# Kernel tuning notes

Measured on AMD Instinct MI355X. Metric: run time of the kernel, lower is better.

The kernel has to match this reference:

```python
import jax, jax.numpy as jnp
import numpy as np
from jax import lax

B, T, D, I, K = 16, 2048, 512, 1024, 31

def setup_inputs() -> dict:
    key = jax.random.key(0)
    ks = jax.random.split(key, 5)
    x = jax.random.normal(ks[0], (B, T, D), dtype=jnp.float32)
    ln_g = jnp.ones((D,), jnp.float32)
    ln_b = jnp.zeros((D,), jnp.float32)
    w1 = jax.random.normal(ks[1], (2 * I, D), dtype=jnp.float32) * 0.02
    b1 = jnp.zeros((2 * I,), jnp.float32)
    dw = jax.random.normal(ks[2], (I, 1, K), dtype=jnp.float32) * 0.1
    dwb = jnp.zeros((I,), jnp.float32)
    alpha = jnp.full((I,), 0.25, jnp.float32)  # PReLU default init
    w2 = jax.random.normal(ks[3], (D, I), dtype=jnp.float32) * 0.02
    b2 = jnp.zeros((D,), jnp.float32)
    return {"x": x, "ln_g": ln_g, "ln_b": ln_b, "w1": w1, "b1": b1,
            "dw": dw, "dwb": dwb, "alpha": alpha, "w2": w2, "b2": b2}

def reference(x, ln_g, ln_b, w1, b1, dw, dwb, alpha, w2, b2):
    # LayerNorm over last dim
    mu = jnp.mean(x, axis=-1, keepdims=True)
    var = jnp.mean(jnp.square(x - mu), axis=-1, keepdims=True)
    xn = (x - mu) * lax.rsqrt(var + 1e-5) * ln_g + ln_b
    # pointwise conv D -> 2I (1x1 conv == GEMM over channels)
    h = jnp.einsum('btd,ed->bte', xn, w1) + b1            # [B,T,2I]
    a, g = jnp.split(h, 2, axis=-1)                       # chunk on channel dim
    u = a * jax.nn.silu(g)                                # SwiGLU [B,T,I]
    # depthwise conv, kernel 31, same padding 15
    uc = jnp.transpose(u, (0, 2, 1))                      # [B,I,T]
    pad = K // 2
    v = lax.conv_general_dilated(uc, dw, window_strides=(1,),
                                 padding=[(pad, pad)],
                                 dimension_numbers=('NCH', 'OIH', 'NCH'),
                                 feature_group_count=I)
    v = v + dwb[None, :, None]
    # PReLU per channel
    v = jnp.where(v > 0, v, alpha[None, :, None] * v)
    # pointwise conv I -> D, then back to [B,T,D]
    out = jnp.einsum('bct,dc->btd', v, w2) + b2
    return out
```

## Files before the change

### kernel.cpp

```cpp
#include <hip/hip_runtime.h>
#include <hip/hip_bf16.h>
#include <stdint.h>

#define B_  16
#define T_  2048
#define D_  512
#define I_  1024
#define K_  31
#define M_  (B_ * T_)

typedef __attribute__((ext_vector_type(8))) __bf16 bf16x8;
typedef __attribute__((ext_vector_type(4))) float  f32x4;

__device__ __forceinline__ unsigned short f2bf(float f) {
    union { float f; uint32_t u; } v; v.f = f;
    uint32_t u = v.u;
    uint32_t r = (u + 0x7FFFu + ((u >> 16) & 1u)) >> 16;
    return (unsigned short)r;
}
__device__ __forceinline__ float bf2f(unsigned short h) {
    union { uint32_t u; float f; } v; v.u = ((uint32_t)h) << 16;
    return v.f;
}

__device__ __forceinline__ void gload_lds16(const void* g, void* l) {
    __builtin_amdgcn_global_load_lds(
        (const __attribute__((address_space(1))) unsigned int*)g,
        (__attribute__((address_space(3))) unsigned int*)l, 16, 0, 0);
}

__global__ __launch_bounds__(256) void prep_weights(
    const float* __restrict__ w1, const float* __restrict__ w2,
    unsigned short* __restrict__ w1b, unsigned short* __restrict__ w2b)
{
    int i = blockIdx.x * 256 + threadIdx.x;
    const int n1 = 2 * I_ * D_;
    const int n2 = D_ * I_;
    if (i < n1) w1b[i] = f2bf(w1[i]);
    if (i < n2) w2b[i] = f2bf(w2[i]);
}

__global__ __launch_bounds__(256) void ln_kernel(
    const float* __restrict__ x, const float* __restrict__ gam,
    const float* __restrict__ bet, unsigned short* __restrict__ xn)
{
    int row  = blockIdx.x * 4 + (threadIdx.x >> 6);
    int lane = threadIdx.x & 63;
    const float* xr = x + (size_t)row * D_ + lane * 8;
    float4 a0 = *(const float4*)xr;
    float4 a1 = *(const float4*)(xr + 4);
    float xs[8] = {a0.x, a0.y, a0.z, a0.w, a1.x, a1.y, a1.z, a1.w};

    float s = xs[0]+xs[1]+xs[2]+xs[3]+xs[4]+xs[5]+xs[6]+xs[7];
    #pragma unroll
    for (int off = 32; off; off >>= 1) s += __shfl_xor(s, off);
    float mu = s * (1.0f / D_);

    float q = 0.f;
    #pragma unroll
    for (int j = 0; j < 8; ++j) { float d = xs[j] - mu; q += d * d; }
    #pragma unroll
    for (int off = 32; off; off >>= 1) q += __shfl_xor(q, off);
    float rstd = rsqrtf(q * (1.0f / D_) + 1e-5f);

    float4 g0 = *(const float4*)(gam + lane * 8);
    float4 g1 = *(const float4*)(gam + lane * 8 + 4);
    float4 e0 = *(const float4*)(bet + lane * 8);
    float4 e1 = *(const float4*)(bet + lane * 8 + 4);
    float gs[8] = {g0.x, g0.y, g0.z, g0.w, g1.x, g1.y, g1.z, g1.w};
    float bs[8] = {e0.x, e0.y, e0.z, e0.w, e1.x, e1.y, e1.z, e1.w};

    unsigned short o[8];
    #pragma unroll
    for (int j = 0; j < 8; ++j) o[j] = f2bf((xs[j] - mu) * rstd * gs[j] + bs[j]);
    uint4 pk;
    pk.x = (uint32_t)o[0] | ((uint32_t)o[1] << 16);
    pk.y = (uint32_t)o[2] | ((uint32_t)o[3] << 16);
    pk.z = (uint32_t)o[4] | ((uint32_t)o[5] << 16);
    pk.w = (uint32_t)o[6] | ((uint32_t)o[7] << 16);
    *(uint4*)(xn + (size_t)row * D_ + lane * 8) = pk;
}


#define PRE_() do { \
    __builtin_amdgcn_s_barrier(); \
    asm volatile("s_waitcnt lgkmcnt(0)" ::: "memory"); \
    __builtin_amdgcn_sched_barrier(0); \
    __builtin_amdgcn_s_setprio(1); } while (0)

#define POST0_() do { \
    __builtin_amdgcn_s_setprio(0); \
    __builtin_amdgcn_sched_barrier(0); \
    __builtin_amdgcn_s_barrier(); } while (0)

#define POSTV_(six) do { \
    __builtin_amdgcn_s_setprio(0); \
    __builtin_amdgcn_sched_barrier(0); \
    if (six) asm volatile("s_waitcnt vmcnt(6)" ::: "memory"); \
    else     asm volatile("s_waitcnt vmcnt(0)" ::: "memory"); \
    __builtin_amdgcn_s_barrier(); } while (0)

#define POSTW_(two) do { \
    __builtin_amdgcn_s_setprio(0); \
    __builtin_amdgcn_sched_barrier(0); \
    if (two) asm volatile("s_waitcnt vmcnt(2)" ::: "memory"); \
    __builtin_amdgcn_s_barrier(); } while (0)

#define RD(base, idx) (*(const bf16x8*)(lds + (base) + (idx) * 2048))
#define MF(m, n, a, b) \
    acc[m][n] = __builtin_amdgcn_mfma_f32_16x16x32_bf16(a, b, acc[m][n], 0, 0, 0)

#define ISSUE_A(j, c) do { \
    gload_lds16(agA[j], lds + (c) * 65536 + tid * 16 + (j) * 8192); \
    agA[j] += 64; } while (0)
#define ISSUE_B(j, c) do { \
    gload_lds16(agB[j], lds + (c) * 65536 + 32768 + tid * 16 + (j) * 8192); \
    agB[j] += 64; } while (0)
#define ISSUE6(c) do { ISSUE_B(0,c); ISSUE_B(1,c); ISSUE_B(2,c); ISSUE_B(3,c); \
                       ISSUE_A(0,c); ISSUE_A(2,c); } while (0)
#define ISSUE2(c) do { ISSUE_A(1,c); ISSUE_A(3,c); } while (0)

#define KTILE(CUR, NXT, DOISS, VM6) do { \
    bf16x8 af0, af1, af2, af3, bb0, bb1, bb2, bb3; \
    bb0 = RD(bB0[CUR],0); bb1 = RD(bB0[CUR],1); bb2 = RD(bB0[CUR],2); bb3 = RD(bB0[CUR],3); \
    af0 = RD(bA0[CUR],0); af1 = RD(bA0[CUR],1); af2 = RD(bA0[CUR],2); af3 = RD(bA0[CUR],3); \
    if (DOISS) { ISSUE6(NXT); } \
    PRE_(); \
    MF(0,0,af0,bb0); MF(0,1,af0,bb1); MF(0,2,af0,bb2); MF(0,3,af0,bb3); \
    MF(1,0,af1,bb0); MF(1,1,af1,bb1); MF(1,2,af1,bb2); MF(1,3,af1,bb3); \
    MF(2,0,af2,bb0); MF(2,1,af2,bb1); MF(2,2,af2,bb2); MF(2,3,af2,bb3); \
    MF(3,0,af3,bb0); MF(3,1,af3,bb1); MF(3,2,af3,bb2); MF(3,3,af3,bb3); \
    POSTV_(VM6); \
    af0 = RD(bA0[CUR],4); af1 = RD(bA0[CUR],5); af2 = RD(bA0[CUR],6); af3 = RD(bA0[CUR],7); \
    if (DOISS) { ISSUE2(NXT); } \
    PRE_(); \
    MF(4,0,af0,bb0); MF(4,1,af0,bb1); MF(4,2,af0,bb2); MF(4,3,af0,bb3); \
    MF(5,0,af1,bb0); MF(5,1,af1,bb1); MF(5,2,af1,bb2); MF(5,3,af1,bb3); \
    MF(6,0,af2,bb0); MF(6,1,af2,bb1); MF(6,2,af2,bb2); MF(6,3,af2,bb3); \
    MF(7,0,af3,bb0); MF(7,1,af3,bb1); MF(7,2,af3,bb2); MF(7,3,af3,bb3); \
    POST0_(); \
    bb0 = RD(bB1[CUR],0); bb1 = RD(bB1[CUR],1); bb2 = RD(bB1[CUR],2); bb3 = RD(bB1[CUR],3); \
    af0 = RD(bA1[CUR],0); af1 = RD(bA1[CUR],1); af2 = RD(bA1[CUR],2); af3 = RD(bA1[CUR],3); \
    PRE_(); \
    MF(0,0,af0,bb0); MF(0,1,af0,bb1); MF(0,2,af0,bb2); MF(0,3,af0,bb3); \
    MF(1,0,af1,bb0); MF(1,1,af1,bb1); MF(1,2,af1,bb2); MF(1,3,af1,bb3); \
    MF(2,0,af2,bb0); MF(2,1,af2,bb1); MF(2,2,af2,bb2); MF(2,3,af2,bb3); \
    MF(3,0,af3,bb0); MF(3,1,af3,bb1); MF(3,2,af3,bb2); MF(3,3,af3,bb3); \
    POST0_(); \
    af0 = RD(bA1[CUR],4); af1 = RD(bA1[CUR],5); af2 = RD(bA1[CUR],6); af3 = RD(bA1[CUR],7); \
    PRE_(); \
    MF(4,0,af0,bb0); MF(4,1,af0,bb1); MF(4,2,af0,bb2); MF(4,3,af0,bb3); \
    MF(5,0,af1,bb0); MF(5,1,af1,bb1); MF(5,2,af1,bb2); MF(5,3,af1,bb3); \
    MF(6,0,af2,bb0); MF(6,1,af2,bb1); MF(6,2,af2,bb2); MF(6,3,af2,bb3); \
    MF(7,0,af3,bb0); MF(7,1,af3,bb1); MF(7,2,af3,bb2); MF(7,3,af3,bb3); \
    POSTW_(DOISS); \
} while (0)

__global__ __launch_bounds__(512, 2) void gemm1_kernel(
    const unsigned short* __restrict__ xn,
    const unsigned short* __restrict__ w1b,
    const float* __restrict__ b1,
    unsigned short* __restrict__ u)
{
    __shared__ __align__(16) unsigned char lds[131072];
    const int tid  = threadIdx.x;
    const int lane = tid & 63;
    const int wv   = tid >> 6;
    const int wm   = wv >> 2;
    const int wn   = wv & 3;

    const int bid = blockIdx.x;
    const int sw  = (bid & 7) * 128 + (bid >> 3);
    const int jb  = sw & 7;
    const int m0  = (sw >> 3) * 256;

    const unsigned short* agA[4];
    const unsigned short* agB[4];
    {
        const int srow = tid >> 3;
        const int scb  = tid & 7;
        #pragma unroll
        for (int j = 0; j < 4; ++j) {
            int row = j * 64 + srow;
            int kk  = (scb ^ (row & 7)) * 8;
            agA[j] = xn + (size_t)(m0 + row) * D_ + kk;
            int chl  = ((row >> 5) << 4) + (row & 15);
            int wrow = ((row & 16) ? 1024 : 0) + jb * 128 + chl;
            agB[j] = w1b + (size_t)wrow * D_ + kk;
        }
    }

    const int l15 = lane & 15;
    const unsigned kq  = (unsigned)((lane >> 4) << 4);
    const unsigned swx = (unsigned)((l15 & 7) << 4);
    const unsigned rA  = (unsigned)(wm * 128 + l15) * 128;
    const unsigned rB  = 32768u + (unsigned)(wn * 64 + l15) * 128;
    const unsigned bA0[2] = {rA + (kq ^ swx),          rA + (kq ^ swx) + 65536u};
    const unsigned bA1[2] = {rA + ((64u + kq) ^ swx),  rA + ((64u + kq) ^ swx) + 65536u};
    const unsigned bB0[2] = {rB + (kq ^ swx),          rB + (kq ^ swx) + 65536u};
    const unsigned bB1[2] = {rB + ((64u + kq) ^ swx),  rB + ((64u + kq) ^ swx) + 65536u};

    f32x4 acc[8][4];
    #pragma unroll
    for (int i = 0; i < 8; ++i)
        #pragma unroll
        for (int n = 0; n < 4; ++n) acc[i][n] = (f32x4){0.f, 0.f, 0.f, 0.f};

    ISSUE6(0); ISSUE2(0);
    asm volatile("s_waitcnt vmcnt(2)" ::: "memory");
    __builtin_amdgcn_s_barrier();

    const int NT = D_ / 64;
    for (int tt = 0; tt < NT; tt += 2) {
        KTILE(0, 1, true, true);
        const bool more = (tt + 2 < NT);
        KTILE(1, 0, more, more);
    }

    const int rQ = (lane >> 4) * 4;
    #pragma unroll
    for (int p = 0; p < 2; ++p) {
        int ch = jb * 128 + wn * 32 + p * 16 + l15;
        float ba = b1[ch];
        float bg = b1[1024 + ch];
        #pragma unroll
        for (int mf = 0; mf < 8; ++mf) {
            #pragma unroll
            for (int r = 0; r < 4; ++r) {
                float a = acc[mf][2 * p][r] + ba;
                float g = acc[mf][2 * p + 1][r] + bg;
                float sg = g / (1.0f + __expf(-g));
                int row = m0 + wm * 128 + mf * 16 + rQ + r;
                u[(size_t)row * I_ + ch] = f2bf(a * sg);
            }
        }
    }
}

__global__ __launch_bounds__(256) void dwconv_kernel(
    const unsigned short* __restrict__ u, const float* __restrict__ dw,
    const float* __restrict__ dwb, const float* __restrict__ alpha,
    unsigned short* __restrict__ v)
{
    __shared__ __align__(16) unsigned short su[286][64];
    const int tid     = threadIdx.x;
    const int c0      = blockIdx.y * 64;
    const int b       = blockIdx.z;
    const int tile_t0 = blockIdx.x * 256;

    #pragma unroll
    for (int it = 0; it < 9; ++it) {
        int r = it * 32 + (tid >> 3);
        if (r < 286) {
            int tt = tile_t0 - 15 + r;
            int cc = (tid & 7) * 8;
            uint4 val = {0u, 0u, 0u, 0u};
            if (tt >= 0 && tt < T_)
                val = *(const uint4*)(u + ((size_t)b * T_ + tt) * I_ + c0 + cc);
            *(uint4*)(&su[r][cc]) = val;
        }
    }
    __syncthreads();

    const int c  = tid & 63;
    const int tb = (tid >> 6) * 64;

    float dwk[K_];
    #pragma unroll
    for (int k = 0; k < K_; ++k) dwk[k] = dw[(c0 + c) * K_ + k];
    const float bia = dwb[c0 + c], al = alpha[c0 + c];

    unsigned short* vb = v + ((size_t)b * T_ + tile_t0 + tb) * I_ + c0 + c;

    #pragma unroll
    for (int chk = 0; chk < 4; ++chk) {
        float w[46];
        #pragma unroll
        for (int j = 0; j < 46; ++j)
            w[j] = bf2f(su[tb + chk * 16 + j][c]);
        #pragma unroll
        for (int i = 0; i < 16; ++i) {
            float acc = bia;
            #pragma unroll
            for (int k = 0; k < K_; ++k) acc += w[i + k] * dwk[k];
            float o = acc > 0.f ? acc : al * acc;
            vb[(size_t)(chk * 16 + i) * I_] = f2bf(o);
        }
    }
}

__global__ __launch_bounds__(512, 2) void gemm2_kernel(
    const unsigned short* __restrict__ v,
    const unsigned short* __restrict__ w2b,
    const float* __restrict__ b2,
    float* __restrict__ out)
{
    __shared__ __align__(16) unsigned char lds[131072];
    const int tid  = threadIdx.x;
    const int lane = tid & 63;
    const int wv   = tid >> 6;
    const int wm   = wv >> 2;
    const int wn   = wv & 3;

    const int bid = blockIdx.x;
    const int sw  = (bid & 7) * 32 + (bid >> 3);
    const int n0  = (sw & 1) * 256;
    const int m0  = (sw >> 1) * 256;

    const unsigned short* agA[4];
    const unsigned short* agB[4];
    {
        const int srow = tid >> 3;
        const int scb  = tid & 7;
        #pragma unroll
        for (int j = 0; j < 4; ++j) {
            int row = j * 64 + srow;
            int kk  = (scb ^ (row & 7)) * 8;
            agA[j] = v   + (size_t)(m0 + row) * I_ + kk;
            agB[j] = w2b + (size_t)(n0 + row) * I_ + kk;
        }
    }

    const int l15 = lane & 15;
    const unsigned kq  = (unsigned)((lane >> 4) << 4);
    const unsigned swx = (unsigned)((l15 & 7) << 4);
    const unsigned rA  = (unsigned)(wm * 128 + l15) * 128;
    const unsigned rB  = 32768u + (unsigned)(wn * 64 + l15) * 128;
    const unsigned bA0[2] = {rA + (kq ^ swx),          rA + (kq ^ swx) + 65536u};
    const unsigned bA1[2] = {rA + ((64u + kq) ^ swx),  rA + ((64u + kq) ^ swx) + 65536u};
    const unsigned bB0[2] = {rB + (kq ^ swx),          rB + (kq ^ swx) + 65536u};
    const unsigned bB1[2] = {rB + ((64u + kq) ^ swx),  rB + ((64u + kq) ^ swx) + 65536u};

    f32x4 acc[8][4];
    #pragma unroll
    for (int i = 0; i < 8; ++i)
        #pragma unroll
        for (int n = 0; n < 4; ++n) acc[i][n] = (f32x4){0.f, 0.f, 0.f, 0.f};

    ISSUE6(0); ISSUE2(0);
    asm volatile("s_waitcnt vmcnt(2)" ::: "memory");
    __builtin_amdgcn_s_barrier();

    const int NT = I_ / 64;
    for (int tt = 0; tt < NT; tt += 2) {
        KTILE(0, 1, true, true);
        const bool more = (tt + 2 < NT);
        KTILE(1, 0, more, more);
    }

    const int rQ = (lane >> 4) * 4;
    #pragma unroll
    for (int nf = 0; nf < 4; ++nf) {
        int col = n0 + wn * 64 + nf * 16 + l15;
        float bb = b2[col];
        #pragma unroll
        for (int mf = 0; mf < 8; ++mf) {
            #pragma unroll
            for (int r = 0; r < 4; ++r) {
                int row = m0 + wm * 128 + mf * 16 + rQ + r;
                out[(size_t)row * D_ + col] = acc[mf][nf][r] + bb;
            }
        }
    }
}

extern "C" void kernel_launch(void* const* d_in, const int* in_sizes, int n_in,
                              void* d_out, int out_size, void* d_ws, size_t ws_size,
                              hipStream_t stream) {
    const float* x     = (const float*)d_in[0];
    const float* ln_g  = (const float*)d_in[1];
    const float* ln_b  = (const float*)d_in[2];
    const float* w1    = (const float*)d_in[3];
    const float* b1    = (const float*)d_in[4];
    const float* dw    = (const float*)d_in[5];
    const float* dwb   = (const float*)d_in[6];
    const float* alpha = (const float*)d_in[7];
    const float* w2    = (const float*)d_in[8];
    const float* b2    = (const float*)d_in[9];
    float* out = (float*)d_out;

    char* ws = (char*)d_ws;
    unsigned short* xn  = (unsigned short*)(ws);
    unsigned short* u   = (unsigned short*)(ws + 33554432);
    unsigned short* v   = (unsigned short*)(ws + 100663296);
    unsigned short* w1b = (unsigned short*)(ws + 167772160);
    unsigned short* w2b = (unsigned short*)(ws + 169869312);

    prep_weights<<<4096, 256, 0, stream>>>(w1, w2, w1b, w2b);
    ln_kernel<<<M_ / 4, 256, 0, stream>>>(x, ln_g, ln_b, xn);
    gemm1_kernel<<<(M_ / 256) * (I_ / 128), 512, 0, stream>>>(xn, w1b, b1, u);
    dim3 gc(T_ / 256, I_ / 64, B_);
    dwconv_kernel<<<gc, 256, 0, stream>>>(u, dw, dwb, alpha, v);
    gemm2_kernel<<<(M_ / 256) * (D_ / 256), 512, 0, stream>>>(v, w2b, b2, out);
}
```

Baseline: 214.6 us.

## Make GEMM kernels persistent over output tiles and drop intra-tile barriers

gemm1 now launches 256 blocks, and each block loops over four output column tiles. The global-to-LDS prefetch of the next tile's K slices is issued during the current tile's last steps, so loads run across tile boundaries. Inside each K-tile the per-quarter s_barrier calls are removed, leaving only two barriers per K-tile, and the SiLU divide is replaced with a hardware reciprocal. This cuts launch and prologue overhead and synchronization stalls, at the risk of LDS read/write races from the reduced barriers and fewer blocks for load balance.

```diff
diff --git a/kernel.cpp b/kernel.cpp
--- a/kernel.cpp
+++ b/kernel.cpp
@@ -82,33 +82,17 @@
 }
 
 
-#define PRE_() do { \
-    __builtin_amdgcn_s_barrier(); \
-    asm volatile("s_waitcnt lgkmcnt(0)" ::: "memory"); \
-    __builtin_amdgcn_sched_barrier(0); \
-    __builtin_amdgcn_s_setprio(1); } while (0)
-
-#define POST0_() do { \
-    __builtin_amdgcn_s_setprio(0); \
-    __builtin_amdgcn_sched_barrier(0); \
-    __builtin_amdgcn_s_barrier(); } while (0)
-
-#define POSTV_(six) do { \
-    __builtin_amdgcn_s_setprio(0); \
-    __builtin_amdgcn_sched_barrier(0); \
-    if (six) asm volatile("s_waitcnt vmcnt(6)" ::: "memory"); \
-    else     asm volatile("s_waitcnt vmcnt(0)" ::: "memory"); \
-    __builtin_amdgcn_s_barrier(); } while (0)
-
-#define POSTW_(two) do { \
-    __builtin_amdgcn_s_setprio(0); \
-    __builtin_amdgcn_sched_barrier(0); \
-    if (two) asm volatile("s_waitcnt vmcnt(2)" ::: "memory"); \
-    __builtin_amdgcn_s_barrier(); } while (0)
+#define VMCNT(n) asm volatile("s_waitcnt vmcnt(" #n ")" ::: "memory")
 
 #define RD(base, idx) (*(const bf16x8*)(lds + (base) + (idx) * 2048))
 #define MF(m, n, a, b) \
     acc[m][n] = __builtin_amdgcn_mfma_f32_16x16x32_bf16(a, b, acc[m][n], 0, 0, 0)
+#define MFQ(MB, x0, x1, x2, x3, c0, c1, c2, c3) do { \
+    MF(MB+0,0,x0,c0); MF(MB+0,1,x0,c1); MF(MB+0,2,x0,c2); MF(MB+0,3,x0,c3); \
+    MF(MB+1,0,x1,c0); MF(MB+1,1,x1,c1); MF(MB+1,2,x1,c2); MF(MB+1,3,x1,c3); \
+    MF(MB+2,0,x2,c0); MF(MB+2,1,x2,c1); MF(MB+2,2,x2,c2); MF(MB+2,3,x2,c3); \
+    MF(MB+3,0,x3,c0); MF(MB+3,1,x3,c1); MF(MB+3,2,x3,c2); MF(MB+3,3,x3,c3); \
+} while (0)
 
 #define ISSUE_A(j, c) do { \
     gload_lds16(agA[j], lds + (c) * 65536 + tid * 16 + (j) * 8192); \
@@ -120,40 +104,38 @@
                        ISSUE_A(0,c); ISSUE_A(2,c); } while (0)
 #define ISSUE2(c) do { ISSUE_A(1,c); ISSUE_A(3,c); } while (0)
 
-#define KTILE(CUR, NXT, DOISS, VM6) do { \
-    bf16x8 af0, af1, af2, af3, bb0, bb1, bb2, bb3; \
-    bb0 = RD(bB0[CUR],0); bb1 = RD(bB0[CUR],1); bb2 = RD(bB0[CUR],2); bb3 = RD(bB0[CUR],3); \
-    af0 = RD(bA0[CUR],0); af1 = RD(bA0[CUR],1); af2 = RD(bA0[CUR],2); af3 = RD(bA0[CUR],3); \
+#define LGKM_SCHED() do { \
+    asm volatile("s_waitcnt lgkmcnt(0)" ::: "memory"); \
+    __builtin_amdgcn_sched_barrier(0); } while (0)
+
+#define KTILE2(CUR, NXT, DOISS) do { \
+    bf16x8 b0,b1,b2,b3, x0,x1,x2,x3; \
+    b0 = RD(bB0[CUR],0); b1 = RD(bB0[CUR],1); b2 = RD(bB0[CUR],2); b3 = RD(bB0[CUR],3); \
+    x0 = RD(bA0[CUR],0); x1 = RD(bA0[CUR],1); x2 = RD(bA0[CUR],2); x3 = RD(bA0[CUR],3); \
     if (DOISS) { ISSUE6(NXT); } \
-    PRE_(); \
-    MF(0,0,af0,bb0); MF(0,1,af0,bb1); MF(0,2,af0,bb2); MF(0,3,af0,bb3); \
-    MF(1,0,af1,bb0); MF(1,1,af1,bb1); MF(1,2,af1,bb2); MF(1,3,af1,bb3); \
-    MF(2,0,af2,bb0); MF(2,1,af2,bb1); MF(2,2,af2,bb2); MF(2,3,af2,bb3); \
-    MF(3,0,af3,bb0); MF(3,1,af3,bb1); MF(3,2,af3,bb2); MF(3,3,af3,bb3); \
-    POSTV_(VM6); \
-    af0 = RD(bA0[CUR],4); af1 = RD(bA0[CUR],5); af2 = RD(bA0[CUR],6); af3 = RD(bA0[CUR],7); \
+    __builtin_amdgcn_s_setprio(1); \
+    MFQ(0, x0,x1,x2,x3, b0,b1,b2,b3); \
+    __builtin_amdgcn_s_setprio(0); \
+    LGKM_SCHED(); \
+    if (DOISS) { VMCNT(6); } else { VMCNT(0); } \
+    __builtin_amdgcn_s_barrier(); \
+    x0 = RD(bA0[CUR],4); x1 = RD(bA0[CUR],5); x2 = RD(bA0[CUR],6); x3 = RD(bA0[CUR],7); \
     if (DOISS) { ISSUE2(NXT); } \
-    PRE_(); \
-    MF(4,0,af0,bb0); MF(4,1,af0,bb1); MF(4,2,af0,bb2); MF(4,3,af0,bb3); \
-    MF(5,0,af1,bb0); MF(5,1,af1,bb1); MF(5,2,af1,bb2); MF(5,3,af1,bb3); \
-    MF(6,0,af2,bb0); MF(6,1,af2,bb1); MF(6,2,af2,bb2); MF(6,3,af2,bb3); \
-    MF(7,0,af3,bb0); MF(7,1,af3,bb1); MF(7,2,af3,bb2); MF(7,3,af3,bb3); \
-    POST0_(); \
-    bb0 = RD(bB1[CUR],0); bb1 = RD(bB1[CUR],1); bb2 = RD(bB1[CUR],2); bb3 = RD(bB1[CUR],3); \
-    af0 = RD(bA1[CUR],0); af1 = RD(bA1[CUR],1); af2 = RD(bA1[CUR],2); af3 = RD(bA1[CUR],3); \
-    PRE_(); \
-    MF(0,0,af0,bb0); MF(0,1,af0,bb1); MF(0,2,af0,bb2); MF(0,3,af0,bb3); \
-    MF(1,0,af1,bb0); MF(1,1,af1,bb1); MF(1,2,af1,bb2); MF(1,3,af1,bb3); \
-    MF(2,0,af2,bb0); MF(2,1,af2,bb1); MF(2,2,af2,bb2); MF(2,3,af2,bb3); \
-    MF(3,0,af3,bb0); MF(3,1,af3,bb1); MF(3,2,af3,bb2); MF(3,3,af3,bb3); \
-    POST0_(); \
-    af0 = RD(bA1[CUR],4); af1 = RD(bA1[CUR],5); af2 = RD(bA1[CUR],6); af3 = RD(bA1[CUR],7); \
-    PRE_(); \
-    MF(4,0,af0,bb0); MF(4,1,af0,bb1); MF(4,2,af0,bb2); MF(4,3,af0,bb3); \
-    MF(5,0,af1,bb0); MF(5,1,af1,bb1); MF(5,2,af1,bb2); MF(5,3,af1,bb3); \
-    MF(6,0,af2,bb0); MF(6,1,af2,bb1); MF(6,2,af2,bb2); MF(6,3,af2,bb3); \
-    MF(7,0,af3,bb0); MF(7,1,af3,bb1); MF(7,2,af3,bb2); MF(7,3,af3,bb3); \
-    POSTW_(DOISS); \
+    __builtin_amdgcn_s_setprio(1); \
+    MFQ(4, x0,x1,x2,x3, b0,b1,b2,b3); \
+    __builtin_amdgcn_s_setprio(0); \
+    b0 = RD(bB1[CUR],0); b1 = RD(bB1[CUR],1); b2 = RD(bB1[CUR],2); b3 = RD(bB1[CUR],3); \
+    x0 = RD(bA1[CUR],0); x1 = RD(bA1[CUR],1); x2 = RD(bA1[CUR],2); x3 = RD(bA1[CUR],3); \
+    __builtin_amdgcn_s_setprio(1); \
+    MFQ(0, x0,x1,x2,x3, b0,b1,b2,b3); \
+    __builtin_amdgcn_s_setprio(0); \
+    x0 = RD(bA1[CUR],4); x1 = RD(bA1[CUR],5); x2 = RD(bA1[CUR],6); x3 = RD(bA1[CUR],7); \
+    __builtin_amdgcn_s_setprio(1); \
+    MFQ(4, x0,x1,x2,x3, b0,b1,b2,b3); \
+    __builtin_amdgcn_s_setprio(0); \
+    LGKM_SCHED(); \
+    if (DOISS) { VMCNT(2); } \
+    __builtin_amdgcn_s_barrier(); \
 } while (0)
 
 __global__ __launch_bounds__(512, 2) void gemm1_kernel(
@@ -170,9 +152,9 @@
     const int wn   = wv & 3;
 
     const int bid = blockIdx.x;
-    const int sw  = (bid & 7) * 128 + (bid >> 3);
-    const int jb  = sw & 7;
-    const int m0  = (sw >> 3) * 256;
+    const int sw  = (bid & 7) * 32 + (bid >> 3);
+    const int m0  = (sw >> 1) * 256;
+    const int jbg = sw & 1;
 
     const unsigned short* agA[4];
     const unsigned short* agB[4];
@@ -185,7 +167,7 @@
             int kk  = (scb ^ (row & 7)) * 8;
             agA[j] = xn + (size_t)(m0 + row) * D_ + kk;
             int chl  = ((row >> 5) << 4) + (row & 15);
-            int wrow = ((row & 16) ? 1024 : 0) + jb * 128 + chl;
+            int wrow = ((row & 16) ? 1024 : 0) + jbg * 512 + chl;
             agB[j] = w1b + (size_t)wrow * D_ + kk;
         }
     }
@@ -207,33 +189,46 @@
         for (int n = 0; n < 4; ++n) acc[i][n] = (f32x4){0.f, 0.f, 0.f, 0.f};
 
     ISSUE6(0); ISSUE2(0);
-    asm volatile("s_waitcnt vmcnt(2)" ::: "memory");
+    VMCNT(2);
     __builtin_amdgcn_s_barrier();
 
-    const int NT = D_ / 64;
-    for (int tt = 0; tt < NT; tt += 2) {
-        KTILE(0, 1, true, true);
-        const bool more = (tt + 2 < NT);
-        KTILE(1, 0, more, more);
-    }
-
     const int rQ = (lane >> 4) * 4;
-    #pragma unroll
-    for (int p = 0; p < 2; ++p) {
-        int ch = jb * 128 + wn * 32 + p * 16 + l15;
-        float ba = b1[ch];
-        float bg = b1[1024 + ch];
-        #pragma unroll
-        for (int mf = 0; mf < 8; ++mf) {
-            #pragma unroll
-            for (int r = 0; r < 4; ++r) {
-                float a = acc[mf][2 * p][r] + ba;
-                float g = acc[mf][2 * p + 1][r] + bg;
-                float sg = g / (1.0f + __expf(-g));
-                int row = m0 + wm * 128 + mf * 16 + rQ + r;
-                u[(size_t)row * I_ + ch] = f2bf(a * sg);
+    for (int ot = 0; ot < 4; ++ot) {
+        const bool more = (ot < 3);
+        #pragma unroll 1
+        for (int h = 0; h < 3; ++h) {
+            KTILE2(0, 1, true);
+            KTILE2(1, 0, true);
+        }
+        KTILE2(0, 1, true);
+        if (more) {
+            #pragma unroll
+            for (int j = 0; j < 4; ++j) { agA[j] -= 512; agB[j] += 65536 - 512; }
+        }
+        KTILE2(1, 0, more);
+
+        const int jb = jbg * 4 + ot;
+        #pragma unroll
+        for (int p = 0; p < 2; ++p) {
+            int ch = jb * 128 + wn * 32 + p * 16 + l15;
+            float ba = b1[ch];
+            float bg = b1[1024 + ch];
+            #pragma unroll
+            for (int mf = 0; mf < 8; ++mf) {
+                #pragma unroll
+                for (int r = 0; r < 4; ++r) {
+                    float a = acc[mf][2 * p][r] + ba;
+                    float g = acc[mf][2 * p + 1][r] + bg;
+                    float sg = g * __builtin_amdgcn_rcpf(1.0f + __expf(-g));
+                    int row = m0 + wm * 128 + mf * 16 + rQ + r;
+                    u[(size_t)row * I_ + ch] = f2bf(a * sg);
+                }
             }
         }
+        #pragma unroll
+        for (int i = 0; i < 8; ++i)
+            #pragma unroll
+            for (int n = 0; n < 4; ++n) acc[i][n] = (f32x4){0.f, 0.f, 0.f, 0.f};
     }
 }
 
@@ -338,15 +333,16 @@
         for (int n = 0; n < 4; ++n) acc[i][n] = (f32x4){0.f, 0.f, 0.f, 0.f};
 
     ISSUE6(0); ISSUE2(0);
-    asm volatile("s_waitcnt vmcnt(2)" ::: "memory");
+    VMCNT(2);
     __builtin_amdgcn_s_barrier();
 
-    const int NT = I_ / 64;
-    for (int tt = 0; tt < NT; tt += 2) {
-        KTILE(0, 1, true, true);
-        const bool more = (tt + 2 < NT);
-        KTILE(1, 0, more, more);
-    }
+    #pragma unroll 1
+    for (int h = 0; h < 7; ++h) {
+        KTILE2(0, 1, true);
+        KTILE2(1, 0, true);
+    }
+    KTILE2(0, 1, true);
+    KTILE2(1, 0, false);
 
     const int rQ = (lane >> 4) * 4;
     #pragma unroll
@@ -388,8 +384,8 @@
 
     prep_weights<<<4096, 256, 0, stream>>>(w1, w2, w1b, w2b);
     ln_kernel<<<M_ / 4, 256, 0, stream>>>(x, ln_g, ln_b, xn);
-    gemm1_kernel<<<(M_ / 256) * (I_ / 128), 512, 0, stream>>>(xn, w1b, b1, u);
+    gemm1_kernel<<<256, 512, 0, stream>>>(xn, w1b, b1, u);
     dim3 gc(T_ / 256, I_ / 64, B_);
     dwconv_kernel<<<gc, 256, 0, stream>>>(u, dw, dwb, alpha, v);
-    gemm2_kernel<<<(M_ / 256) * (D_ / 256), 512, 0, stream>>>(v, w2b, b2, out);
-}
+    gemm2_kernel<<<256, 512, 0, stream>>>(v, w2b, b2, out);
+}
```

Result: slower. 248.8 us (+16.0%).
